# Performance work log

Hardware: AMD Instinct MI355X
Metric: run time of the kernel (lower is better)

## Reference

```python
import jax, jax.numpy as jnp
import numpy as np
from jax import lax

T, H = 4096, 2048          # tokens, hidden_size
E, K = 64, 8               # n_routed_experts, top_k
I = 512                    # moe_intermediate_size
IS = 512                   # shared intermediate = moe_intermediate_size * n_shared_experts
ROUTED_SCALING = 2.5


def setup_inputs() -> dict:
    key = jax.random.key(0)
    ks = jax.random.split(key, 6)
    return {
        "hidden_states": jax.random.normal(ks[0], (T, H), jnp.float32),
        "gate_w": jax.random.normal(ks[1], (H, E), jnp.float32) * 0.05,
        "w13": jax.random.normal(ks[2], (E, H, 2 * I), jnp.float32) * 0.02,
        "w2": jax.random.normal(ks[3], (E, I, H), jnp.float32) * 0.02,
        "shared_w13": jax.random.normal(ks[4], (H, 2 * IS), jnp.float32) * 0.02,
        "shared_w2": jax.random.normal(ks[5], (IS, H), jnp.float32) * 0.02,
    }


def reference(hidden_states, gate_w, w13, w2, shared_w13, shared_w2):
    # --- router: sigmoid scoring, grouped top-k with 1 group == plain top-k ---
    logits = hidden_states @ gate_w                        # [T, E]
    scores = jax.nn.sigmoid(logits.astype(jnp.float32))
    topk_w, topk_ids = lax.top_k(scores, K)                # [T, K]
    topk_w = topk_w / jnp.sum(topk_w, axis=-1, keepdims=True)  # renormalize

    # --- dispatch: sort token-expert pairs by expert id, grouped GEMM ---
    flat_ids = topk_ids.reshape(-1)                        # [T*K]
    order = jnp.argsort(flat_ids)                          # pairs grouped by expert
    token_idx = order // K                                 # source token of each sorted pair
    x_sorted = hidden_states[token_idx]                    # [T*K, H]
    group_sizes = jnp.bincount(flat_ids, length=E).astype(jnp.int32)

    gu = lax.ragged_dot(x_sorted, w13, group_sizes)        # [T*K, 2I]
    h = jax.nn.silu(gu[:, :I]) * gu[:, I:]                 # SiluAndMul
    out_sorted = lax.ragged_dot(h, w2, group_sizes)        # [T*K, H]

    # --- combine: unsort, weight, sum over top-k ---
    inv = jnp.argsort(order)
    out_pairs = out_sorted[inv].reshape(T, K, H)
    routed = jnp.sum(out_pairs * topk_w[..., None].astype(out_pairs.dtype), axis=1)

    # --- shared expert MLP ---
    sg = hidden_states @ shared_w13                        # [T, 2*IS]
    shared = (jax.nn.silu(sg[:, :IS]) * sg[:, IS:]) @ shared_w2

    return routed * ROUTED_SCALING + shared
```

## Files before the change

kernel.cpp:

```cpp
#include <hip/hip_runtime.h>
#include <hip/hip_bf16.h>

#define T_TOK 4096
#define HD    2048
#define NE    64
#define TOPK  8
#define IMID  512
#define N13   1024
#define NPAIR (T_TOK*TOPK)
#define NROWS (NPAIR + T_TOK)
#define MAXT2 208
#define RSCALE 2.5f

typedef __attribute__((ext_vector_type(8))) __bf16 bf16x8;
typedef __attribute__((ext_vector_type(4))) float  f32x4;

__global__ __launch_bounds__(256) void init_kernel(float4* __restrict__ out4,
                                                   int* __restrict__ counts,
                                                   int* __restrict__ curs) {
  int gid = blockIdx.x * 256 + threadIdx.x;
  float4 z; z.x = z.y = z.z = z.w = 0.f;
  out4[gid] = z;
  if (gid < NE + 1) { counts[gid] = 0; curs[gid] = 0; }
}

__global__ __launch_bounds__(256) void cvt_kernel(const float4* __restrict__ hs4,
                                                  bf16x8* __restrict__ hb8) {
  int gid = blockIdx.x * 256 + threadIdx.x;
  float4 a = hs4[2 * gid], b = hs4[2 * gid + 1];
  bf16x8 v = { (__bf16)a.x, (__bf16)a.y, (__bf16)a.z, (__bf16)a.w,
               (__bf16)b.x, (__bf16)b.y, (__bf16)b.z, (__bf16)b.w };
  hb8[gid] = v;
}

__global__ __launch_bounds__(256) void logits_kernel(const float* __restrict__ hs,
                                                     const float* __restrict__ gw,
                                                     float* __restrict__ logits) {
  __shared__ float hsm[64][16];
  __shared__ float gwm[64][64];
  int tid = threadIdx.x;
  int tb = blockIdx.x * 16;
  int tok = tid >> 4, e4 = (tid & 15) * 4;
  float acc[4] = {0.f, 0.f, 0.f, 0.f};
  for (int c = 0; c < 32; ++c) {
    int kb = c * 64;
    {
      int t16 = tid & 15, kq = tid >> 4;
      float4 f = *(const float4*)&hs[(size_t)(tb + t16) * HD + kb + kq * 4];
      hsm[kq * 4 + 0][t16] = f.x; hsm[kq * 4 + 1][t16] = f.y;
      hsm[kq * 4 + 2][t16] = f.z; hsm[kq * 4 + 3][t16] = f.w;
#pragma unroll
      for (int it = 0; it < 4; ++it) {
        int q = tid + it * 256;
        int gr = q >> 4, gc = (q & 15) * 4;
        *(float4*)&gwm[gr][gc] = *(const float4*)&gw[(size_t)(kb + gr) * NE + gc];
      }
    }
    __syncthreads();
#pragma unroll 8
    for (int k = 0; k < 64; ++k) {
      float h = hsm[k][tok];
      float4 g = *(const float4*)&gwm[k][e4];
      acc[0] += h * g.x; acc[1] += h * g.y; acc[2] += h * g.z; acc[3] += h * g.w;
    }
    __syncthreads();
  }
#pragma unroll
  for (int j = 0; j < 4; ++j) logits[(size_t)(tb + tok) * NE + e4 + j] = acc[j];
}

__global__ __launch_bounds__(256) void top8_kernel(const float* __restrict__ logits,
                                                   int* __restrict__ topk_id,
                                                   float* __restrict__ pair_w,
                                                   int* __restrict__ counts) {
  int lane = threadIdx.x & 63;
  int t = blockIdx.x * 4 + (threadIdx.x >> 6);
  float v = logits[(size_t)t * NE + lane];
  float s = 1.f / (1.f + __expf(-v));
  float cur = s, ssum = 0.f;
  int myid = 0; float myw = 0.f;
  for (int k = 0; k < TOPK; ++k) {
    float bv = cur; int bi = lane;
#pragma unroll
    for (int off = 32; off >= 1; off >>= 1) {
      float ov = __shfl_xor(bv, off);
      int   oi = __shfl_xor(bi, off);
      if (ov > bv || (ov == bv && oi < bi)) { bv = ov; bi = oi; }
    }
    ssum += bv;
    if (lane == k) { myid = bi; myw = bv; }
    if (lane == bi) cur = -1.f;
  }
  if (lane < TOPK) {
    topk_id[(size_t)t * TOPK + lane] = myid;
    pair_w[(size_t)t * TOPK + lane] = myw / ssum * RSCALE;
    atomicAdd(&counts[myid], 1);
  }
}

__global__ void scan_kernel(const int* __restrict__ counts, int* __restrict__ offs,
                            int2* __restrict__ tiles) {
  __shared__ int cnt[65], pref[66], tp[66];
  int tid = threadIdx.x;
  if (tid < 64) cnt[tid] = counts[tid];
  if (tid == 64) cnt[64] = T_TOK;
  __syncthreads();
  if (tid == 0) {
    int o = 0, t = 0;
    for (int e = 0; e <= 64; ++e) {
      pref[e] = o; tp[e] = t;
      o += cnt[e]; t += (cnt[e] + 255) >> 8;
    }
    pref[65] = o; tp[65] = t;
  }
  __syncthreads();
  if (tid <= 64) {
    offs[tid] = pref[tid];
    int c = cnt[tid], base = pref[tid], tb = tp[tid];
    int nt = (c + 255) >> 8;
    for (int i = 0; i < nt; ++i) {
      int rr = c - i * 256; if (rr > 256) rr = 256;
      tiles[tb + i] = make_int2(base + i * 256, (tid << 16) | rr);
    }
  }
  __syncthreads();
  for (int i = tp[65] + tid; i < MAXT2; i += 128) tiles[i] = make_int2(0, 0);
}

__global__ __launch_bounds__(256) void scatter_kernel(const int* __restrict__ topk_id,
                                                      const float* __restrict__ pair_w,
                                                      const int* __restrict__ offs,
                                                      int* __restrict__ curs,
                                                      int* __restrict__ row_token,
                                                      float* __restrict__ row_w) {
  int p = blockIdx.x * 256 + threadIdx.x;
  int dst, t; float w;
  if (p < NPAIR) {
    t = p >> 3; int e = topk_id[p]; w = pair_w[p];
    dst = offs[e] + atomicAdd(&curs[e], 1);
  } else {
    t = p - NPAIR; w = 1.0f;
    dst = NPAIR + t;
  }
  row_token[dst] = t;
  row_w[dst] = w;
}

__device__ __forceinline__ int swz(int row, int kbyte) {
  return row * 128 + (kbyte ^ ((row & 7) << 4));
}
__device__ __forceinline__ void glds16(const void* g, void* l) {
  __builtin_amdgcn_global_load_lds((const __attribute__((address_space(1))) void*)g,
                                   (__attribute__((address_space(3))) void*)l, 16, 0, 0);
}
__device__ __forceinline__ void store_bx8(__bf16* Bs, int col, int kbyte, const float* p) {
  bf16x8 v = { (__bf16)p[0], (__bf16)p[1], (__bf16)p[2], (__bf16)p[3],
               (__bf16)p[4], (__bf16)p[5], (__bf16)p[6], (__bf16)p[7] };
  *(bf16x8*)&Bs[swz(col, kbyte) >> 1] = v;
}

__global__ __launch_bounds__(1024, 4) void gemm1_kernel(const __bf16* __restrict__ hidden_bf,
                                                        const float* __restrict__ w13,
                                                        const float* __restrict__ sw13,
                                                        const int* __restrict__ row_token,
                                                        const int2* __restrict__ tiles,
                                                        __bf16* __restrict__ hbuf) {
  int2 td = tiles[blockIdx.y];
  int rows = td.y & 0xFFFF;
  if (rows == 0) return;
  int e = td.y >> 16, row0 = td.x;
  const float* W = (e < NE) ? (w13 + (size_t)e * (HD * N13)) : sw13;
  int n0 = blockIdx.x * 64;

  __shared__ __bf16 As[2][256 * 64];
  __shared__ __bf16 Bgs[2][64 * 64];
  __shared__ __bf16 Bus[2][64 * 64];

  int tid = threadIdx.x;
  int lane = tid & 63, wv = tid >> 6;
  int wrow = wv >> 1, wc = wv & 1;
  int l15 = lane & 15, lq = lane >> 4;

  int kswz = (((lane & 7) ^ ((lane >> 3) & 7)) << 3);
  const __bf16* Abase[2];
#pragma unroll
  for (int i = 0; i < 2; ++i) {
    int grow = row0 + wv * 16 + i * 8 + (lane >> 3);
    if (grow >= NROWS) grow = NROWS - 1;
    Abase[i] = hidden_bf + (size_t)row_token[grow] * HD + kswz;
  }
  int bm = tid >> 9, bcol = tid & 63, bkq = (tid >> 6) & 7;
  const float* Bp0 = W + (size_t)(bkq * 8) * N13 + n0 + bm * 512 + bcol;
  __bf16* Bmy[2];
  Bmy[0] = bm ? Bus[0] : Bgs[0];
  Bmy[1] = bm ? Bus[1] : Bgs[1];

  float p[8];
#pragma unroll
  for (int r = 0; r < 8; ++r) p[r] = Bp0[(size_t)r * N13];
#pragma unroll
  for (int i = 0; i < 2; ++i) glds16(Abase[i], &As[0][wv * 1024 + i * 512]);
  store_bx8(Bmy[0], bcol, bkq * 16, p);
  asm volatile("s_waitcnt vmcnt(0) lgkmcnt(0)" ::: "memory");
  __builtin_amdgcn_s_barrier();
  __builtin_amdgcn_sched_barrier(0);

  f32x4 accg[2][2], accu[2][2];
#pragma unroll
  for (int i = 0; i < 2; ++i)
#pragma unroll
    for (int j = 0; j < 2; ++j) { accg[i][j] = (f32x4)(0.f); accu[i][j] = (f32x4)(0.f); }

  for (int s = 0; s < 32; ++s) {
    int cur = s & 1;
    if (s + 1 < 32) {
      const float* Bp2 = Bp0 + (size_t)(s + 1) * 64 * N13;
#pragma unroll
      for (int r = 0; r < 8; ++r) p[r] = Bp2[(size_t)r * N13];
    }
    __builtin_amdgcn_sched_barrier(0);
    if (s + 1 < 32) {
#pragma unroll
      for (int i = 0; i < 2; ++i)
        glds16(Abase[i] + (s + 1) * 64, &As[cur ^ 1][wv * 1024 + i * 512]);
    }
    __builtin_amdgcn_sched_barrier(0);
#pragma unroll
    for (int kk = 0; kk < 2; ++kk) {
      int koff = kk * 64 + lq * 16;
      bf16x8 a[2], bg[2], bu[2];
#pragma unroll
      for (int i = 0; i < 2; ++i)
        a[i] = *(const bf16x8*)&As[cur][swz(wrow * 32 + i * 16 + l15, koff) >> 1];
#pragma unroll
      for (int j = 0; j < 2; ++j) {
        bg[j] = *(const bf16x8*)&Bgs[cur][swz(wc * 32 + j * 16 + l15, koff) >> 1];
        bu[j] = *(const bf16x8*)&Bus[cur][swz(wc * 32 + j * 16 + l15, koff) >> 1];
      }
#pragma unroll
      for (int i = 0; i < 2; ++i)
#pragma unroll
        for (int j = 0; j < 2; ++j) {
          accg[i][j] = __builtin_amdgcn_mfma_f32_16x16x32_bf16(a[i], bg[j], accg[i][j], 0, 0, 0);
          accu[i][j] = __builtin_amdgcn_mfma_f32_16x16x32_bf16(a[i], bu[j], accu[i][j], 0, 0, 0);
        }
    }
    if (s + 1 < 32)
      store_bx8(Bmy[cur ^ 1], bcol, bkq * 16, p);
    asm volatile("s_waitcnt vmcnt(0) lgkmcnt(0)" ::: "memory");
    __builtin_amdgcn_s_barrier();
    __builtin_amdgcn_sched_barrier(0);
  }
#pragma unroll
  for (int mi = 0; mi < 2; ++mi) {
#pragma unroll
    for (int r = 0; r < 4; ++r) {
      int rl = wrow * 32 + mi * 16 + lq * 4 + r;
      if (rl < rows) {
        size_t hrow = (size_t)(row0 + rl) * IMID;
#pragma unroll
        for (int j = 0; j < 2; ++j) {
          float g = accg[mi][j][r], u = accu[mi][j][r];
          float hv = g * u / (1.f + __expf(-g));
          hbuf[hrow + n0 + wc * 32 + j * 16 + l15] = (__bf16)hv;
        }
      }
    }
  }
}

__global__ __launch_bounds__(1024, 4) void gemm2_kernel(const __bf16* __restrict__ hbuf,
                                                        const float* __restrict__ w2,
                                                        const float* __restrict__ sw2,
                                                        const int* __restrict__ row_token,
                                                        const float* __restrict__ row_w,
                                                        const int2* __restrict__ tiles,
                                                        float* __restrict__ out) {
  int2 td = tiles[blockIdx.y];
  int rows = td.y & 0xFFFF;
  if (rows == 0) return;
  int e = td.y >> 16, row0 = td.x;
  const float* W = (e < NE) ? (w2 + (size_t)e * (IMID * HD)) : sw2;
  int n0 = blockIdx.x * 128;

  __shared__ __bf16 As[2][256 * 64];
  __shared__ __bf16 Bs[2][128 * 64];

  int tid = threadIdx.x;
  int lane = tid & 63, wv = tid >> 6;
  int wr = wv >> 2, wc = wv & 3;
  int l15 = lane & 15, lq = lane >> 4;

  int kswz = (((lane & 7) ^ ((lane >> 3) & 7)) << 3);
  const __bf16* Abase[2];
#pragma unroll
  for (int i = 0; i < 2; ++i) {
    int grow = row0 + wv * 16 + i * 8 + (lane >> 3);
    if (grow >= NROWS) grow = NROWS - 1;
    Abase[i] = hbuf + (size_t)grow * IMID + kswz;
  }
  int bcol = tid & 127, bkq = tid >> 7;
  const float* Bp0 = W + (size_t)(bkq * 8) * HD + n0 + bcol;

  float p[8];
#pragma unroll
  for (int r = 0; r < 8; ++r) p[r] = Bp0[(size_t)r * HD];
#pragma unroll
  for (int i = 0; i < 2; ++i) glds16(Abase[i], &As[0][wv * 1024 + i * 512]);
  store_bx8(Bs[0], bcol, bkq * 16, p);
  asm volatile("s_waitcnt vmcnt(0) lgkmcnt(0)" ::: "memory");
  __builtin_amdgcn_s_barrier();
  __builtin_amdgcn_sched_barrier(0);

  f32x4 acc[4][2];
#pragma unroll
  for (int i = 0; i < 4; ++i)
#pragma unroll
    for (int j = 0; j < 2; ++j) acc[i][j] = (f32x4)(0.f);

  for (int s = 0; s < 8; ++s) {
    int cur = s & 1;
    if (s + 1 < 8) {
      const float* Bp2 = Bp0 + (size_t)(s + 1) * 64 * HD;
#pragma unroll
      for (int r = 0; r < 8; ++r) p[r] = Bp2[(size_t)r * HD];
    }
    __builtin_amdgcn_sched_barrier(0);
    if (s + 1 < 8) {
#pragma unroll
      for (int i = 0; i < 2; ++i)
        glds16(Abase[i] + (s + 1) * 64, &As[cur ^ 1][wv * 1024 + i * 512]);
    }
    __builtin_amdgcn_sched_barrier(0);
#pragma unroll
    for (int kk = 0; kk < 2; ++kk) {
      int koff = kk * 64 + lq * 16;
      bf16x8 a[4], b[2];
#pragma unroll
      for (int i = 0; i < 4; ++i)
        a[i] = *(const bf16x8*)&As[cur][swz(wr * 64 + i * 16 + l15, koff) >> 1];
#pragma unroll
      for (int j = 0; j < 2; ++j)
        b[j] = *(const bf16x8*)&Bs[cur][swz(wc * 32 + j * 16 + l15, koff) >> 1];
#pragma unroll
      for (int i = 0; i < 4; ++i)
#pragma unroll
        for (int j = 0; j < 2; ++j)
          acc[i][j] = __builtin_amdgcn_mfma_f32_16x16x32_bf16(a[i], b[j], acc[i][j], 0, 0, 0);
    }
    if (s + 1 < 8)
      store_bx8(Bs[cur ^ 1], bcol, bkq * 16, p);
    asm volatile("s_waitcnt vmcnt(0) lgkmcnt(0)" ::: "memory");
    __builtin_amdgcn_s_barrier();
    __builtin_amdgcn_sched_barrier(0);
  }
#pragma unroll
  for (int i = 0; i < 4; ++i) {
#pragma unroll
    for (int r = 0; r < 4; ++r) {
      int rl = wr * 64 + i * 16 + lq * 4 + r;
      if (rl < rows) {
        int gr = row0 + rl;
        int tok = row_token[gr];
        float wgt = row_w[gr];
        float* orow = out + (size_t)tok * HD + n0 + wc * 32;
#pragma unroll
        for (int j = 0; j < 2; ++j)
          atomicAdd(&orow[j * 16 + l15], acc[i][j][r] * wgt);
      }
    }
  }
}

extern "C" void kernel_launch(void* const* d_in, const int* in_sizes, int n_in,
                              void* d_out, int out_size, void* d_ws, size_t ws_size,
                              hipStream_t stream) {
  const float* hidden = (const float*)d_in[0];
  const float* gate_w = (const float*)d_in[1];
  const float* w13    = (const float*)d_in[2];
  const float* w2     = (const float*)d_in[3];
  const float* sw13   = (const float*)d_in[4];
  const float* sw2    = (const float*)d_in[5];
  float* out = (float*)d_out;

  char* ws = (char*)d_ws;
  size_t off = 0;
  __bf16* hbuf      = (__bf16*)(ws + off); off += (size_t)NROWS * IMID * 2;
  __bf16* hidden_bf = (__bf16*)(ws + off); off += (size_t)T_TOK * HD * 2;
  float* logits  = (float*)(ws + off);  off += (size_t)T_TOK * NE * 4;
  int*   topk_id = (int*)(ws + off);    off += (size_t)NPAIR * 4;
  float* pair_w  = (float*)(ws + off);  off += (size_t)NPAIR * 4;
  int*   row_tok = (int*)(ws + off);    off += (size_t)NROWS * 4;
  float* row_w   = (float*)(ws + off);  off += (size_t)NROWS * 4;
  int*   counts  = (int*)(ws + off);    off += 512;
  int*   curs    = (int*)(ws + off);    off += 512;
  int*   offs    = (int*)(ws + off);    off += 512;
  int2*  tiles   = (int2*)(ws + off);   off += MAXT2 * 8;

  init_kernel<<<T_TOK * HD / 4 / 256, 256, 0, stream>>>((float4*)out, counts, curs);
  cvt_kernel<<<T_TOK * HD / 8 / 256, 256, 0, stream>>>((const float4*)hidden, (bf16x8*)hidden_bf);
  logits_kernel<<<T_TOK / 16, 256, 0, stream>>>(hidden, gate_w, logits);
  top8_kernel<<<T_TOK / 4, 256, 0, stream>>>(logits, topk_id, pair_w, counts);
  scan_kernel<<<1, 128, 0, stream>>>(counts, offs, tiles);
  scatter_kernel<<<NROWS / 256, 256, 0, stream>>>(topk_id, pair_w, offs, curs, row_tok, row_w);
  gemm1_kernel<<<dim3(8, MAXT2), 1024, 0, stream>>>(hidden_bf, w13, sw13, row_tok, tiles, hbuf);
  gemm2_kernel<<<dim3(16, MAXT2), 1024, 0, stream>>>(hbuf, w2, sw2, row_tok, row_w, tiles, out);
}
```

Baseline: 848.7 us.

## Halve GEMM block size, single-buffer A, replace atomic combine with gather pass

Both grouped GEMMs drop from 1024 to 512 threads per block, with each wave covering more output columns, and the A tile goes from double to single buffering. Each B thread now loads 16 rows, and s_setprio is raised around the MFMA section. The A load for the next step now waits behind an extra barrier after the compute. When workspace allows, gemm2 writes weighted per-pair rows in bf16 and a combine kernel sums the eight pairs plus the shared row per token with plain stores. This removes the fp32 atomics and the output zeroing, but adds an extra pass over the buffer and bf16 rounding of the partial results.

```diff
diff --git a/kernel.cpp b/kernel.cpp
--- a/kernel.cpp
+++ b/kernel.cpp
@@ -12,25 +12,25 @@
 #define MAXT2 208
 #define RSCALE 2.5f
 
-typedef __attribute__((ext_vector_type(8))) __bf16 bf16x8;
-typedef __attribute__((ext_vector_type(4))) float  f32x4;
-
-__global__ __launch_bounds__(256) void init_kernel(float4* __restrict__ out4,
-                                                   int* __restrict__ counts,
-                                                   int* __restrict__ curs) {
+typedef __attribute__((ext_vector_type(8)))  __bf16 bf16x8;
+typedef __attribute__((ext_vector_type(4)))  float  f32x4;
+
+
+__global__ void init_small(int* __restrict__ counts, int* __restrict__ curs) {
+  int tid = threadIdx.x;
+  if (tid < NE + 1) { counts[tid] = 0; curs[tid] = 0; }
+}
+__global__ __launch_bounds__(256) void zero_out_kernel(float4* __restrict__ out4) {
+  out4[blockIdx.x * 256 + threadIdx.x] = float4{0.f, 0.f, 0.f, 0.f};
+}
+
+__global__ __launch_bounds__(256) void cvt_kernel(const float4* __restrict__ src4,
+                                                  bf16x8* __restrict__ dst8) {
   int gid = blockIdx.x * 256 + threadIdx.x;
-  float4 z; z.x = z.y = z.z = z.w = 0.f;
-  out4[gid] = z;
-  if (gid < NE + 1) { counts[gid] = 0; curs[gid] = 0; }
-}
-
-__global__ __launch_bounds__(256) void cvt_kernel(const float4* __restrict__ hs4,
-                                                  bf16x8* __restrict__ hb8) {
-  int gid = blockIdx.x * 256 + threadIdx.x;
-  float4 a = hs4[2 * gid], b = hs4[2 * gid + 1];
+  float4 a = src4[2 * gid], b = src4[2 * gid + 1];
   bf16x8 v = { (__bf16)a.x, (__bf16)a.y, (__bf16)a.z, (__bf16)a.w,
                (__bf16)b.x, (__bf16)b.y, (__bf16)b.z, (__bf16)b.w };
-  hb8[gid] = v;
+  dst8[gid] = v;
 }
 
 __global__ __launch_bounds__(256) void logits_kernel(const float* __restrict__ hs,
@@ -132,12 +132,14 @@
                                                       const int* __restrict__ offs,
                                                       int* __restrict__ curs,
                                                       int* __restrict__ row_token,
-                                                      float* __restrict__ row_w) {
+                                                      float* __restrict__ row_w,
+                                                      int* __restrict__ inv8) {
   int p = blockIdx.x * 256 + threadIdx.x;
   int dst, t; float w;
   if (p < NPAIR) {
     t = p >> 3; int e = topk_id[p]; w = pair_w[p];
     dst = offs[e] + atomicAdd(&curs[e], 1);
+    inv8[p] = dst;
   } else {
     t = p - NPAIR; w = 1.0f;
     dst = NPAIR + t;
@@ -159,12 +161,12 @@
   *(bf16x8*)&Bs[swz(col, kbyte) >> 1] = v;
 }
 
-__global__ __launch_bounds__(1024, 4) void gemm1_kernel(const __bf16* __restrict__ hidden_bf,
-                                                        const float* __restrict__ w13,
-                                                        const float* __restrict__ sw13,
-                                                        const int* __restrict__ row_token,
-                                                        const int2* __restrict__ tiles,
-                                                        __bf16* __restrict__ hbuf) {
+__global__ __launch_bounds__(512, 2) void gemm1_kernel(const __bf16* __restrict__ hidden_bf,
+                                                       const float* __restrict__ w13,
+                                                       const float* __restrict__ sw13,
+                                                       const int* __restrict__ row_token,
+                                                       const int2* __restrict__ tiles,
+                                                       __bf16* __restrict__ hbuf) {
   int2 td = tiles[blockIdx.y];
   int rows = td.y & 0xFFFF;
   if (rows == 0) return;
@@ -172,81 +174,86 @@
   const float* W = (e < NE) ? (w13 + (size_t)e * (HD * N13)) : sw13;
   int n0 = blockIdx.x * 64;
 
-  __shared__ __bf16 As[2][256 * 64];
+  __shared__ __bf16 As[256 * 64];
   __shared__ __bf16 Bgs[2][64 * 64];
   __shared__ __bf16 Bus[2][64 * 64];
 
   int tid = threadIdx.x;
   int lane = tid & 63, wv = tid >> 6;
-  int wrow = wv >> 1, wc = wv & 1;
   int l15 = lane & 15, lq = lane >> 4;
 
   int kswz = (((lane & 7) ^ ((lane >> 3) & 7)) << 3);
-  const __bf16* Abase[2];
-#pragma unroll
-  for (int i = 0; i < 2; ++i) {
-    int grow = row0 + wv * 16 + i * 8 + (lane >> 3);
+  const __bf16* Abase[4];
+#pragma unroll
+  for (int i = 0; i < 4; ++i) {
+    int grow = row0 + wv * 32 + i * 8 + (lane >> 3);
     if (grow >= NROWS) grow = NROWS - 1;
     Abase[i] = hidden_bf + (size_t)row_token[grow] * HD + kswz;
   }
-  int bm = tid >> 9, bcol = tid & 63, bkq = (tid >> 6) & 7;
-  const float* Bp0 = W + (size_t)(bkq * 8) * N13 + n0 + bm * 512 + bcol;
-  __bf16* Bmy[2];
-  Bmy[0] = bm ? Bus[0] : Bgs[0];
-  Bmy[1] = bm ? Bus[1] : Bgs[1];
-
-  float p[8];
-#pragma unroll
-  for (int r = 0; r < 8; ++r) p[r] = Bp0[(size_t)r * N13];
-#pragma unroll
-  for (int i = 0; i < 2; ++i) glds16(Abase[i], &As[0][wv * 1024 + i * 512]);
-  store_bx8(Bmy[0], bcol, bkq * 16, p);
+  int bm = tid >> 8, bcol = tid & 63, bkq = (tid >> 6) & 3;
+  const float* Bp0 = W + (size_t)(bkq * 16) * N13 + (bm ? 512 + n0 : n0) + bcol;
+
+  float pN[16];
+#pragma unroll
+  for (int r = 0; r < 16; ++r) pN[r] = Bp0[(size_t)r * N13];
+#pragma unroll
+  for (int i = 0; i < 4; ++i) glds16(Abase[i], &As[wv * 2048 + i * 512]);
+  {
+    __bf16* Bmy = bm ? Bus[0] : Bgs[0];
+    store_bx8(Bmy, bcol, bkq * 32, pN);
+    store_bx8(Bmy, bcol, bkq * 32 + 16, pN + 8);
+  }
   asm volatile("s_waitcnt vmcnt(0) lgkmcnt(0)" ::: "memory");
   __builtin_amdgcn_s_barrier();
   __builtin_amdgcn_sched_barrier(0);
 
-  f32x4 accg[2][2], accu[2][2];
+  f32x4 accg[2][4], accu[2][4];
 #pragma unroll
   for (int i = 0; i < 2; ++i)
 #pragma unroll
-    for (int j = 0; j < 2; ++j) { accg[i][j] = (f32x4)(0.f); accu[i][j] = (f32x4)(0.f); }
+    for (int j = 0; j < 4; ++j) { accg[i][j] = (f32x4)(0.f); accu[i][j] = (f32x4)(0.f); }
 
   for (int s = 0; s < 32; ++s) {
     int cur = s & 1;
     if (s + 1 < 32) {
-      const float* Bp2 = Bp0 + (size_t)(s + 1) * 64 * N13;
-#pragma unroll
-      for (int r = 0; r < 8; ++r) p[r] = Bp2[(size_t)r * N13];
-    }
-    __builtin_amdgcn_sched_barrier(0);
-    if (s + 1 < 32) {
-#pragma unroll
-      for (int i = 0; i < 2; ++i)
-        glds16(Abase[i] + (s + 1) * 64, &As[cur ^ 1][wv * 1024 + i * 512]);
-    }
-    __builtin_amdgcn_sched_barrier(0);
+      const float* Bn = Bp0 + (size_t)(s + 1) * 64 * N13;
+#pragma unroll
+      for (int r = 0; r < 16; ++r) pN[r] = Bn[(size_t)r * N13];
+    }
+    __builtin_amdgcn_sched_barrier(0);
+    __builtin_amdgcn_s_setprio(1);
 #pragma unroll
     for (int kk = 0; kk < 2; ++kk) {
       int koff = kk * 64 + lq * 16;
-      bf16x8 a[2], bg[2], bu[2];
+      bf16x8 a[2], bg[4], bu[4];
 #pragma unroll
       for (int i = 0; i < 2; ++i)
-        a[i] = *(const bf16x8*)&As[cur][swz(wrow * 32 + i * 16 + l15, koff) >> 1];
-#pragma unroll
-      for (int j = 0; j < 2; ++j) {
-        bg[j] = *(const bf16x8*)&Bgs[cur][swz(wc * 32 + j * 16 + l15, koff) >> 1];
-        bu[j] = *(const bf16x8*)&Bus[cur][swz(wc * 32 + j * 16 + l15, koff) >> 1];
+        a[i] = *(const bf16x8*)&As[swz(wv * 32 + i * 16 + l15, koff) >> 1];
+#pragma unroll
+      for (int j = 0; j < 4; ++j) {
+        bg[j] = *(const bf16x8*)&Bgs[cur][swz(j * 16 + l15, koff) >> 1];
+        bu[j] = *(const bf16x8*)&Bus[cur][swz(j * 16 + l15, koff) >> 1];
       }
 #pragma unroll
       for (int i = 0; i < 2; ++i)
 #pragma unroll
-        for (int j = 0; j < 2; ++j) {
+        for (int j = 0; j < 4; ++j) {
           accg[i][j] = __builtin_amdgcn_mfma_f32_16x16x32_bf16(a[i], bg[j], accg[i][j], 0, 0, 0);
           accu[i][j] = __builtin_amdgcn_mfma_f32_16x16x32_bf16(a[i], bu[j], accu[i][j], 0, 0, 0);
         }
     }
-    if (s + 1 < 32)
-      store_bx8(Bmy[cur ^ 1], bcol, bkq * 16, p);
+    __builtin_amdgcn_s_setprio(0);
+    __builtin_amdgcn_sched_barrier(0);
+    __builtin_amdgcn_s_barrier();
+    __builtin_amdgcn_sched_barrier(0);
+    if (s + 1 < 32) {
+#pragma unroll
+      for (int i = 0; i < 4; ++i)
+        glds16(Abase[i] + (s + 1) * 64, &As[wv * 2048 + i * 512]);
+      __bf16* Bmy = bm ? Bus[cur ^ 1] : Bgs[cur ^ 1];
+      store_bx8(Bmy, bcol, bkq * 32, pN);
+      store_bx8(Bmy, bcol, bkq * 32 + 16, pN + 8);
+    }
     asm volatile("s_waitcnt vmcnt(0) lgkmcnt(0)" ::: "memory");
     __builtin_amdgcn_s_barrier();
     __builtin_amdgcn_sched_barrier(0);
@@ -255,27 +262,28 @@
   for (int mi = 0; mi < 2; ++mi) {
 #pragma unroll
     for (int r = 0; r < 4; ++r) {
-      int rl = wrow * 32 + mi * 16 + lq * 4 + r;
+      int rl = wv * 32 + mi * 16 + lq * 4 + r;
       if (rl < rows) {
         size_t hrow = (size_t)(row0 + rl) * IMID;
 #pragma unroll
-        for (int j = 0; j < 2; ++j) {
+        for (int j = 0; j < 4; ++j) {
           float g = accg[mi][j][r], u = accu[mi][j][r];
           float hv = g * u / (1.f + __expf(-g));
-          hbuf[hrow + n0 + wc * 32 + j * 16 + l15] = (__bf16)hv;
+          hbuf[hrow + n0 + j * 16 + l15] = (__bf16)hv;
         }
       }
     }
   }
 }
 
-__global__ __launch_bounds__(1024, 4) void gemm2_kernel(const __bf16* __restrict__ hbuf,
-                                                        const float* __restrict__ w2,
-                                                        const float* __restrict__ sw2,
-                                                        const int* __restrict__ row_token,
-                                                        const float* __restrict__ row_w,
-                                                        const int2* __restrict__ tiles,
-                                                        float* __restrict__ out) {
+template<int MODE>
+__global__ __launch_bounds__(512, 2) void gemm2_kernel(const __bf16* __restrict__ hbuf,
+                                                       const float* __restrict__ w2,
+                                                       const float* __restrict__ sw2,
+                                                       const int* __restrict__ row_token,
+                                                       const float* __restrict__ row_w,
+                                                       const int2* __restrict__ tiles,
+                                                       void* __restrict__ dstv) {
   int2 td = tiles[blockIdx.y];
   int rows = td.y & 0xFFFF;
   if (rows == 0) return;
@@ -283,93 +291,127 @@
   const float* W = (e < NE) ? (w2 + (size_t)e * (IMID * HD)) : sw2;
   int n0 = blockIdx.x * 128;
 
-  __shared__ __bf16 As[2][256 * 64];
+  __shared__ __bf16 As[256 * 64];
   __shared__ __bf16 Bs[2][128 * 64];
 
   int tid = threadIdx.x;
   int lane = tid & 63, wv = tid >> 6;
-  int wr = wv >> 2, wc = wv & 3;
+  int wrow = wv >> 1, wc = wv & 1;
   int l15 = lane & 15, lq = lane >> 4;
 
   int kswz = (((lane & 7) ^ ((lane >> 3) & 7)) << 3);
-  const __bf16* Abase[2];
-#pragma unroll
-  for (int i = 0; i < 2; ++i) {
-    int grow = row0 + wv * 16 + i * 8 + (lane >> 3);
+  const __bf16* Abase[4];
+#pragma unroll
+  for (int i = 0; i < 4; ++i) {
+    int grow = row0 + wv * 32 + i * 8 + (lane >> 3);
     if (grow >= NROWS) grow = NROWS - 1;
     Abase[i] = hbuf + (size_t)grow * IMID + kswz;
   }
   int bcol = tid & 127, bkq = tid >> 7;
-  const float* Bp0 = W + (size_t)(bkq * 8) * HD + n0 + bcol;
-
-  float p[8];
-#pragma unroll
-  for (int r = 0; r < 8; ++r) p[r] = Bp0[(size_t)r * HD];
-#pragma unroll
-  for (int i = 0; i < 2; ++i) glds16(Abase[i], &As[0][wv * 1024 + i * 512]);
-  store_bx8(Bs[0], bcol, bkq * 16, p);
+  const float* Bp0 = W + (size_t)(bkq * 16) * HD + n0 + bcol;
+
+  float pN[16];
+#pragma unroll
+  for (int r = 0; r < 16; ++r) pN[r] = Bp0[(size_t)r * HD];
+#pragma unroll
+  for (int i = 0; i < 4; ++i) glds16(Abase[i], &As[wv * 2048 + i * 512]);
+  store_bx8(Bs[0], bcol, bkq * 32, pN);
+  store_bx8(Bs[0], bcol, bkq * 32 + 16, pN + 8);
   asm volatile("s_waitcnt vmcnt(0) lgkmcnt(0)" ::: "memory");
   __builtin_amdgcn_s_barrier();
   __builtin_amdgcn_sched_barrier(0);
 
-  f32x4 acc[4][2];
+  f32x4 acc[4][4];
 #pragma unroll
   for (int i = 0; i < 4; ++i)
 #pragma unroll
-    for (int j = 0; j < 2; ++j) acc[i][j] = (f32x4)(0.f);
+    for (int j = 0; j < 4; ++j) acc[i][j] = (f32x4)(0.f);
 
   for (int s = 0; s < 8; ++s) {
     int cur = s & 1;
     if (s + 1 < 8) {
-      const float* Bp2 = Bp0 + (size_t)(s + 1) * 64 * HD;
-#pragma unroll
-      for (int r = 0; r < 8; ++r) p[r] = Bp2[(size_t)r * HD];
-    }
-    __builtin_amdgcn_sched_barrier(0);
-    if (s + 1 < 8) {
-#pragma unroll
-      for (int i = 0; i < 2; ++i)
-        glds16(Abase[i] + (s + 1) * 64, &As[cur ^ 1][wv * 1024 + i * 512]);
-    }
-    __builtin_amdgcn_sched_barrier(0);
+      const float* Bn = Bp0 + (size_t)(s + 1) * 64 * HD;
+#pragma unroll
+      for (int r = 0; r < 16; ++r) pN[r] = Bn[(size_t)r * HD];
+    }
+    __builtin_amdgcn_sched_barrier(0);
+    __builtin_amdgcn_s_setprio(1);
 #pragma unroll
     for (int kk = 0; kk < 2; ++kk) {
       int koff = kk * 64 + lq * 16;
-      bf16x8 a[4], b[2];
+      bf16x8 a[4], b[4];
 #pragma unroll
       for (int i = 0; i < 4; ++i)
-        a[i] = *(const bf16x8*)&As[cur][swz(wr * 64 + i * 16 + l15, koff) >> 1];
-#pragma unroll
-      for (int j = 0; j < 2; ++j)
-        b[j] = *(const bf16x8*)&Bs[cur][swz(wc * 32 + j * 16 + l15, koff) >> 1];
+        a[i] = *(const bf16x8*)&As[swz(wrow * 64 + i * 16 + l15, koff) >> 1];
+#pragma unroll
+      for (int j = 0; j < 4; ++j)
+        b[j] = *(const bf16x8*)&Bs[cur][swz(wc * 64 + j * 16 + l15, koff) >> 1];
 #pragma unroll
       for (int i = 0; i < 4; ++i)
 #pragma unroll
-        for (int j = 0; j < 2; ++j)
+        for (int j = 0; j < 4; ++j)
           acc[i][j] = __builtin_amdgcn_mfma_f32_16x16x32_bf16(a[i], b[j], acc[i][j], 0, 0, 0);
     }
-    if (s + 1 < 8)
-      store_bx8(Bs[cur ^ 1], bcol, bkq * 16, p);
+    __builtin_amdgcn_s_setprio(0);
+    __builtin_amdgcn_sched_barrier(0);
+    __builtin_amdgcn_s_barrier();
+    __builtin_amdgcn_sched_barrier(0);
+    if (s + 1 < 8) {
+#pragma unroll
+      for (int i = 0; i < 4; ++i)
+        glds16(Abase[i] + (s + 1) * 64, &As[wv * 2048 + i * 512]);
+      store_bx8(Bs[cur ^ 1], bcol, bkq * 32, pN);
+      store_bx8(Bs[cur ^ 1], bcol, bkq * 32 + 16, pN + 8);
+    }
     asm volatile("s_waitcnt vmcnt(0) lgkmcnt(0)" ::: "memory");
     __builtin_amdgcn_s_barrier();
     __builtin_amdgcn_sched_barrier(0);
   }
 #pragma unroll
-  for (int i = 0; i < 4; ++i) {
+  for (int mi = 0; mi < 4; ++mi) {
 #pragma unroll
     for (int r = 0; r < 4; ++r) {
-      int rl = wr * 64 + i * 16 + lq * 4 + r;
+      int rl = wrow * 64 + mi * 16 + lq * 4 + r;
       if (rl < rows) {
         int gr = row0 + rl;
-        int tok = row_token[gr];
         float wgt = row_w[gr];
-        float* orow = out + (size_t)tok * HD + n0 + wc * 32;
-#pragma unroll
-        for (int j = 0; j < 2; ++j)
-          atomicAdd(&orow[j * 16 + l15], acc[i][j][r] * wgt);
+        if (MODE == 1) {
+          __bf16* prow = (__bf16*)dstv + (size_t)gr * HD + n0 + wc * 64;
+#pragma unroll
+          for (int j = 0; j < 4; ++j)
+            prow[j * 16 + l15] = (__bf16)(acc[mi][j][r] * wgt);
+        } else {
+          int tok = row_token[gr];
+          float* orow = (float*)dstv + (size_t)tok * HD + n0 + wc * 64;
+#pragma unroll
+          for (int j = 0; j < 4; ++j)
+            atomicAdd(&orow[j * 16 + l15], acc[mi][j][r] * wgt);
+        }
       }
     }
   }
+}
+
+__global__ __launch_bounds__(256) void combine_kernel(const __bf16* __restrict__ pairout,
+                                                      const int* __restrict__ inv8,
+                                                      float* __restrict__ out) {
+  int t = blockIdx.x;
+  int c = threadIdx.x * 8;
+  float s0 = 0.f, s1 = 0.f, s2 = 0.f, s3 = 0.f, s4 = 0.f, s5 = 0.f, s6 = 0.f, s7 = 0.f;
+#pragma unroll
+  for (int k = 0; k < 8; ++k) {
+    bf16x8 v = *(const bf16x8*)(pairout + (size_t)inv8[t * 8 + k] * HD + c);
+    s0 += (float)v[0]; s1 += (float)v[1]; s2 += (float)v[2]; s3 += (float)v[3];
+    s4 += (float)v[4]; s5 += (float)v[5]; s6 += (float)v[6]; s7 += (float)v[7];
+  }
+  {
+    bf16x8 v = *(const bf16x8*)(pairout + (size_t)(NPAIR + t) * HD + c);
+    s0 += (float)v[0]; s1 += (float)v[1]; s2 += (float)v[2]; s3 += (float)v[3];
+    s4 += (float)v[4]; s5 += (float)v[5]; s6 += (float)v[6]; s7 += (float)v[7];
+  }
+  float4* o = (float4*)(out + (size_t)t * HD + c);
+  o[0] = float4{s0, s1, s2, s3};
+  o[1] = float4{s4, s5, s6, s7};
 }
 
 extern "C" void kernel_launch(void* const* d_in, const int* in_sizes, int n_in,
@@ -392,17 +434,32 @@
   float* pair_w  = (float*)(ws + off);  off += (size_t)NPAIR * 4;
   int*   row_tok = (int*)(ws + off);    off += (size_t)NROWS * 4;
   float* row_w   = (float*)(ws + off);  off += (size_t)NROWS * 4;
+  int*   inv8    = (int*)(ws + off);    off += (size_t)NPAIR * 4;
   int*   counts  = (int*)(ws + off);    off += 512;
   int*   curs    = (int*)(ws + off);    off += 512;
   int*   offs    = (int*)(ws + off);    off += 512;
   int2*  tiles   = (int2*)(ws + off);   off += MAXT2 * 8;
-
-  init_kernel<<<T_TOK * HD / 4 / 256, 256, 0, stream>>>((float4*)out, counts, curs);
+  off = (off + 255) & ~(size_t)255;
+  __bf16* pairout = (__bf16*)(ws + off);
+  size_t need_rows = off + (size_t)NROWS * HD * 2;
+  bool rows_path = (ws_size >= need_rows);
+
+  init_small<<<1, 256, 0, stream>>>(counts, curs);
+  if (!rows_path)
+    zero_out_kernel<<<T_TOK * HD / 4 / 256, 256, 0, stream>>>((float4*)out);
   cvt_kernel<<<T_TOK * HD / 8 / 256, 256, 0, stream>>>((const float4*)hidden, (bf16x8*)hidden_bf);
   logits_kernel<<<T_TOK / 16, 256, 0, stream>>>(hidden, gate_w, logits);
   top8_kernel<<<T_TOK / 4, 256, 0, stream>>>(logits, topk_id, pair_w, counts);
   scan_kernel<<<1, 128, 0, stream>>>(counts, offs, tiles);
-  scatter_kernel<<<NROWS / 256, 256, 0, stream>>>(topk_id, pair_w, offs, curs, row_tok, row_w);
-  gemm1_kernel<<<dim3(8, MAXT2), 1024, 0, stream>>>(hidden_bf, w13, sw13, row_tok, tiles, hbuf);
-  gemm2_kernel<<<dim3(16, MAXT2), 1024, 0, stream>>>(hbuf, w2, sw2, row_tok, row_w, tiles, out);
-}
+  scatter_kernel<<<NROWS / 256, 256, 0, stream>>>(topk_id, pair_w, offs, curs,
+                                                  row_tok, row_w, inv8);
+  gemm1_kernel<<<dim3(8, MAXT2), 512, 0, stream>>>(hidden_bf, w13, sw13, row_tok, tiles, hbuf);
+  if (rows_path) {
+    gemm2_kernel<1><<<dim3(16, MAXT2), 512, 0, stream>>>(hbuf, w2, sw2, row_tok, row_w,
+                                                         tiles, (void*)pairout);
+    combine_kernel<<<T_TOK, 256, 0, stream>>>(pairout, inv8, out);
+  } else {
+    gemm2_kernel<0><<<dim3(16, MAXT2), 512, 0, stream>>>(hbuf, w2, sw2, row_tok, row_w,
+                                                         tiles, (void*)out);
+  }
+}
```

Measured after the change: 804.4 us. 5.2% less time.
